# Kernel optimization log

Hardware: AMD Instinct MI355X
Metric: run time of the kernel (lower is better)

Reference implementation:

```python
import jax, jax.numpy as jnp
import numpy as np

W_DIM = 512
IN_CH = 512
OUT_CH = 512
K = 3
PAD = K // 2
LR_MUL = 1.0
WEIGHT_GAIN = LR_MUL / np.sqrt(IN_CH * K * K)
MOD_WEIGHT_GAIN = 1.0 / np.sqrt(W_DIM)  # EqualizedLinear lr_mul=1.0
MOD_BIAS_GAIN = 1.0


def setup_inputs() -> dict:
    key = jax.random.key(0)
    k1, k2, k3, k4 = jax.random.split(key, 4)
    x = jax.random.normal(k1, (16, IN_CH, 64, 64), dtype=jnp.float32)
    w = jax.random.normal(k2, (16, W_DIM), dtype=jnp.float32)
    weight = jax.random.normal(k3, (OUT_CH, IN_CH, K, K), dtype=jnp.float32) / LR_MUL
    mod_weight = jax.random.normal(k4, (IN_CH, W_DIM), dtype=jnp.float32)
    mod_bias = jnp.ones((IN_CH,), dtype=jnp.float32)  # bias_init=1.0
    return {"x": x, "w": w, "weight": weight, "mod_weight": mod_weight, "mod_bias": mod_bias}


def _conv_one(xi, wi):
    # xi: [C_in, H, W], wi: [C_out, C_in, K, K]
    out = jax.lax.conv_general_dilated(
        xi[None], wi, window_strides=(1, 1),
        padding=[(PAD, PAD), (PAD, PAD)],
        dimension_numbers=("NCHW", "OIHW", "NCHW"))
    return out[0]


def reference(x, w, weight, mod_weight, mod_bias):
    # style = EqualizedLinear(w): [B, C_in]
    style = w @ (mod_weight * MOD_WEIGHT_GAIN).T + mod_bias * MOD_BIAS_GAIN
    # modulate weights per-sample: [B, C_out, C_in, K, K]
    wmod = (weight * WEIGHT_GAIN)[None] * style[:, None, :, None, None]
    # demodulate
    demod = jax.lax.rsqrt(jnp.sum(jnp.square(wmod), axis=(2, 3, 4), keepdims=True) + 1e-8)
    wmod = wmod * demod
    # per-sample conv (groups=batch in the original) via vmap
    out = jax.vmap(_conv_one)(x, wmod)  # [B, C_out, H, W]
    return out
```

## Files before the change

### kernel.cpp

```cpp
#include <hip/hip_runtime.h>
#include <hip/hip_bf16.h>

#define IN_CH 512
#define OUT_CH 512
#define HW 64
#define BATCH 16
#define WEIGHT_GAIN 0.014731391274719739f
#define MOD_WEIGHT_GAIN 0.04419417382415922f

#define PAD_W 66
#define XS_PIX_STRIDE 512

typedef __attribute__((ext_vector_type(8))) short frag8;
typedef __attribute__((ext_vector_type(4))) float f32x4;

__global__ void style_kernel(const float* __restrict__ w, const float* __restrict__ mw,
                             const float* __restrict__ mb, float* __restrict__ style) {
    __shared__ float wsh[512];
    const int b = blockIdx.x;
    const int i = threadIdx.x;
    wsh[i] = w[b * 512 + i];
    __syncthreads();
    const float4* row = (const float4*)(mw + i * 512);
    float s = 0.f;
#pragma unroll 4
    for (int j = 0; j < 128; ++j) {
        float4 v = row[j];
        const float* ws = &wsh[j * 4];
        s += v.x * ws[0] + v.y * ws[1] + v.z * ws[2] + v.w * ws[3];
    }
    style[b * 512 + i] = s * MOD_WEIGHT_GAIN + mb[i];
}

__global__ void wprep_kernel(const float* __restrict__ weight, float* __restrict__ wsq,
                             __hip_bfloat16* __restrict__ wbf) {
    const int idx = blockIdx.x * 256 + threadIdx.x;
    const float* wp = weight + idx * 9;
    float s = 0.f;
#pragma unroll
    for (int kk = 0; kk < 9; ++kk) {
        float v = wp[kk];
        s += v * v;
        wbf[kk * 262144 + idx] = __float2bfloat16(v);
    }
    wsq[idx] = s * (WEIGHT_GAIN * WEIGHT_GAIN);
}

__global__ void demod_kernel(const float* __restrict__ style, const float* __restrict__ wsq,
                             float* __restrict__ sc) {
    __shared__ float s2[512];
    const int b = blockIdx.x;
    const int o = threadIdx.x;
    float st = style[b * 512 + o];
    s2[o] = st * st;
    __syncthreads();
    const float4* row = (const float4*)(wsq + o * 512);
    float acc = 0.f;
#pragma unroll 4
    for (int j = 0; j < 128; ++j) {
        float4 v = row[j];
        const float* ss = &s2[j * 4];
        acc += v.x * ss[0] + v.y * ss[1] + v.z * ss[2] + v.w * ss[3];
    }
    sc[b * 512 + o] = rsqrtf(acc + 1e-8f) * WEIGHT_GAIN;
}

__global__ void xs_kernel(const float* __restrict__ x, const float* __restrict__ style,
                          __hip_bfloat16* __restrict__ xsp) {
    __shared__ float tile[64][65];
    const int y = blockIdx.x;
    const int i0 = blockIdx.y * 64;
    const int b = blockIdx.z;
    const int t = threadIdx.x;

    {
        const int ii = t >> 2;
        const int x0 = (t & 3) * 16;
        const float st = style[b * 512 + i0 + ii];
        const float4* s4 = (const float4*)(x + (((size_t)b * 512 + i0 + ii) * 64 + y) * 64 + x0);
#pragma unroll
        for (int k4 = 0; k4 < 4; ++k4) {
            float4 v = s4[k4];
            float* d = &tile[ii][x0 + k4 * 4];
            d[0] = v.x * st; d[1] = v.y * st; d[2] = v.z * st; d[3] = v.w * st;
        }
    }
    __syncthreads();
    {
        const int xx = t >> 2;
        const int j0 = (t & 3) * 16;
        __hip_bfloat16* dst = xsp + (((size_t)b * PAD_W + (y + 1)) * PAD_W + (xx + 1)) * XS_PIX_STRIDE + i0 + j0;
        union { __hip_bfloat16 h[16]; uint4 u[2]; } pk;
#pragma unroll
        for (int k = 0; k < 16; ++k) pk.h[k] = __float2bfloat16(tile[j0 + k][xx]);
        ((uint4*)dst)[0] = pk.u[0];
        ((uint4*)dst)[1] = pk.u[1];
    }
}

__global__ void conv_kernel(const __hip_bfloat16* __restrict__ wbf,
                            const __hip_bfloat16* __restrict__ xsp,
                            const float* __restrict__ sc,
                            float* __restrict__ out) {
    __shared__ __hip_bfloat16 ash[128 * 64];
    __shared__ __hip_bfloat16 bsh[128 * 64];

    const int t = threadIdx.x;
    const int p0 = blockIdx.x * 128;
    const int m0 = blockIdx.y * 128;
    const int b  = blockIdx.z;
    const int y0 = p0 >> 6;

    const int r_base = t >> 3;
    const int s_slot = (t & 7) ^ (r_base & 7);
    const int aoff = (m0 + r_base) * 512 + s_slot * 8;
    int pixoff[4];
#pragma unroll
    for (int q = 0; q < 4; ++q) {
        const int rB = q * 32 + r_base;
        const int yy = y0 + (rB >> 6);
        const int xx = rB & 63;
        pixoff[q] = (((b * PAD_W) + yy) * PAD_W + xx) * XS_PIX_STRIDE + s_slot * 8;
    }

    const int wv = t >> 6;
    const int wm = (wv >> 1) * 64;
    const int wn = (wv & 1) * 64;
    const int lane = t & 63;
    const int ln15 = lane & 15;
    const int quad = lane >> 4;

    f32x4 acc[4][4] = {};

    const short* ashp = (const short*)ash;
    const short* bshp = (const short*)bsh;

    for (int kk = 0; kk < 9; ++kk) {
        const __hip_bfloat16* wsrc = wbf + kk * 262144 + aoff;
        const int shift = ((kk / 3) * PAD_W + (kk % 3)) * XS_PIX_STRIDE;
        const __hip_bfloat16* xbase = xsp + shift;

        for (int c0 = 0; c0 < 512; c0 += 64) {
#pragma unroll
            for (int q = 0; q < 4; ++q) {
                __builtin_amdgcn_global_load_lds(
                    (const __attribute__((address_space(1))) unsigned int*)(wsrc + q * 16384 + c0),
                    (__attribute__((address_space(3))) unsigned int*)((char*)ash + q * 4096 + t * 16),
                    16, 0, 0);
            }
#pragma unroll
            for (int q = 0; q < 4; ++q) {
                __builtin_amdgcn_global_load_lds(
                    (const __attribute__((address_space(1))) unsigned int*)(xbase + pixoff[q] + c0),
                    (__attribute__((address_space(3))) unsigned int*)((char*)bsh + q * 4096 + t * 16),
                    16, 0, 0);
            }
            __syncthreads();

#pragma unroll
            for (int ks = 0; ks < 2; ++ks) {
                const int gq = ks * 4 + quad;
                frag8 af[4], bfr[4];
#pragma unroll
                for (int mt = 0; mt < 4; ++mt) {
                    const int R = wm + mt * 16 + ln15;
                    af[mt] = *(const frag8*)(ashp + R * 64 + ((gq ^ (R & 7)) << 3));
                }
#pragma unroll
                for (int nt = 0; nt < 4; ++nt) {
                    const int R = wn + nt * 16 + ln15;
                    bfr[nt] = *(const frag8*)(bshp + R * 64 + ((gq ^ (R & 7)) << 3));
                }
#pragma unroll
                for (int mt = 0; mt < 4; ++mt)
#pragma unroll
                    for (int nt = 0; nt < 4; ++nt)
                        acc[mt][nt] = __builtin_amdgcn_mfma_f32_16x16x32_bf16(
                            af[mt], bfr[nt], acc[mt][nt], 0, 0, 0);
            }
            __syncthreads();
        }
    }

    const float* scb = sc + b * 512;
    float* outb = out + (size_t)b * 512 * 4096;
#pragma unroll
    for (int mt = 0; mt < 4; ++mt) {
        const int mrow = m0 + wm + mt * 16 + quad * 4;
#pragma unroll
        for (int v = 0; v < 4; ++v) {
            const float s = scb[mrow + v];
            float* orow = outb + (size_t)(mrow + v) * 4096 + p0 + wn + ln15;
#pragma unroll
            for (int nt = 0; nt < 4; ++nt)
                orow[nt * 16] = acc[mt][nt][v] * s;
        }
    }
}

extern "C" void kernel_launch(void* const* d_in, const int* in_sizes, int n_in,
                              void* d_out, int out_size, void* d_ws, size_t ws_size,
                              hipStream_t stream) {
    (void)in_sizes; (void)n_in; (void)out_size; (void)ws_size;
    const float* x      = (const float*)d_in[0];
    const float* w      = (const float*)d_in[1];
    const float* weight = (const float*)d_in[2];
    const float* mw     = (const float*)d_in[3];
    const float* mb     = (const float*)d_in[4];
    float* out = (float*)d_out;

    char* ws = (char*)d_ws;
    float* style         = (float*)(ws + 0);
    float* sc            = (float*)(ws + 32768);
    float* wsq           = (float*)(ws + 65536);
    __hip_bfloat16* wbf  = (__hip_bfloat16*)(ws + 1114112);
    __hip_bfloat16* xsp  = (__hip_bfloat16*)(ws + 5832704);

    hipMemsetAsync(xsp, 0, (size_t)BATCH * PAD_W * PAD_W * XS_PIX_STRIDE * 2, stream);

    style_kernel<<<dim3(BATCH), dim3(512), 0, stream>>>(w, mw, mb, style);
    wprep_kernel<<<dim3(1024), dim3(256), 0, stream>>>(weight, wsq, wbf);
    demod_kernel<<<dim3(BATCH), dim3(512), 0, stream>>>(style, wsq, sc);
    xs_kernel<<<dim3(64, 8, BATCH), dim3(256), 0, stream>>>(x, style, xsp);
    conv_kernel<<<dim3(32, 4, BATCH), dim3(256), 0, stream>>>(wbf, xsp, sc, out);
}
```

Before: 575.8 us.

## Parallelize prep kernels with wave-per-row reductions and zero only padded border

Style and demod matvecs move from 16 blocks (one thread per output row, serial over 512 inputs) to one wavefront per output with shuffle reductions across 2048 blocks, which spreads the work over the whole GPU. The full-buffer memset of the padded activation tensor is replaced by a small kernel that zeroes only the border pixels. The x-scaling transpose kernel drops its shared-memory tile: each lane handles one pixel, reads 32 channels with strided loads and writes 64 contiguous bytes. The prep phase is latency-bound, so the conv kernel still dominates total time, and the strided uncoalesced-per-lane reads in xs_kernel could hurt.

```diff
diff --git a/kernel.cpp b/kernel.cpp
--- a/kernel.cpp
+++ b/kernel.cpp
@@ -16,20 +16,19 @@
 
 __global__ void style_kernel(const float* __restrict__ w, const float* __restrict__ mw,
                              const float* __restrict__ mb, float* __restrict__ style) {
-    __shared__ float wsh[512];
-    const int b = blockIdx.x;
-    const int i = threadIdx.x;
-    wsh[i] = w[b * 512 + i];
-    __syncthreads();
-    const float4* row = (const float4*)(mw + i * 512);
-    float s = 0.f;
-#pragma unroll 4
-    for (int j = 0; j < 128; ++j) {
-        float4 v = row[j];
-        const float* ws = &wsh[j * 4];
-        s += v.x * ws[0] + v.y * ws[1] + v.z * ws[2] + v.w * ws[3];
-    }
-    style[b * 512 + i] = s * MOD_WEIGHT_GAIN + mb[i];
+    const int gw = (blockIdx.x * 256 + threadIdx.x) >> 6;
+    const int lane = threadIdx.x & 63;
+    const int b = gw >> 9;
+    const int i = gw & 511;
+    const float4* mwp = (const float4*)(mw + (size_t)i * 512 + lane * 8);
+    const float4* wp  = (const float4*)(w + (size_t)b * 512 + lane * 8);
+    float4 m0 = mwp[0], m1 = mwp[1];
+    float4 w0 = wp[0],  w1 = wp[1];
+    float s = m0.x * w0.x + m0.y * w0.y + m0.z * w0.z + m0.w * w0.w
+            + m1.x * w1.x + m1.y * w1.y + m1.z * w1.z + m1.w * w1.w;
+#pragma unroll
+    for (int off = 32; off > 0; off >>= 1) s += __shfl_down(s, off, 64);
+    if (lane == 0) style[(size_t)b * 512 + i] = s * MOD_WEIGHT_GAIN + mb[i];
 }
 
 __global__ void wprep_kernel(const float* __restrict__ weight, float* __restrict__ wsq,
@@ -48,54 +47,55 @@
 
 __global__ void demod_kernel(const float* __restrict__ style, const float* __restrict__ wsq,
                              float* __restrict__ sc) {
-    __shared__ float s2[512];
-    const int b = blockIdx.x;
-    const int o = threadIdx.x;
-    float st = style[b * 512 + o];
-    s2[o] = st * st;
-    __syncthreads();
-    const float4* row = (const float4*)(wsq + o * 512);
-    float acc = 0.f;
-#pragma unroll 4
-    for (int j = 0; j < 128; ++j) {
-        float4 v = row[j];
-        const float* ss = &s2[j * 4];
-        acc += v.x * ss[0] + v.y * ss[1] + v.z * ss[2] + v.w * ss[3];
-    }
-    sc[b * 512 + o] = rsqrtf(acc + 1e-8f) * WEIGHT_GAIN;
+    const int gw = (blockIdx.x * 256 + threadIdx.x) >> 6;
+    const int lane = threadIdx.x & 63;
+    const int b = gw >> 9;
+    const int o = gw & 511;
+    const float4* wq = (const float4*)(wsq + (size_t)o * 512 + lane * 8);
+    const float4* st = (const float4*)(style + (size_t)b * 512 + lane * 8);
+    float4 q0 = wq[0], q1 = wq[1];
+    float4 s0 = st[0], s1 = st[1];
+    float acc = q0.x * s0.x * s0.x + q0.y * s0.y * s0.y + q0.z * s0.z * s0.z + q0.w * s0.w * s0.w
+              + q1.x * s1.x * s1.x + q1.y * s1.y * s1.y + q1.z * s1.z * s1.z + q1.w * s1.w * s1.w;
+#pragma unroll
+    for (int off = 32; off > 0; off >>= 1) acc += __shfl_down(acc, off, 64);
+    if (lane == 0) sc[(size_t)b * 512 + o] = rsqrtf(acc + 1e-8f) * WEIGHT_GAIN;
 }
 
 __global__ void xs_kernel(const float* __restrict__ x, const float* __restrict__ style,
                           __hip_bfloat16* __restrict__ xsp) {
-    __shared__ float tile[64][65];
     const int y = blockIdx.x;
-    const int i0 = blockIdx.y * 64;
     const int b = blockIdx.z;
     const int t = threadIdx.x;
-
-    {
-        const int ii = t >> 2;
-        const int x0 = (t & 3) * 16;
-        const float st = style[b * 512 + i0 + ii];
-        const float4* s4 = (const float4*)(x + (((size_t)b * 512 + i0 + ii) * 64 + y) * 64 + x0);
-#pragma unroll
-        for (int k4 = 0; k4 < 4; ++k4) {
-            float4 v = s4[k4];
-            float* d = &tile[ii][x0 + k4 * 4];
-            d[0] = v.x * st; d[1] = v.y * st; d[2] = v.z * st; d[3] = v.w * st;
-        }
-    }
-    __syncthreads();
-    {
-        const int xx = t >> 2;
-        const int j0 = (t & 3) * 16;
-        __hip_bfloat16* dst = xsp + (((size_t)b * PAD_W + (y + 1)) * PAD_W + (xx + 1)) * XS_PIX_STRIDE + i0 + j0;
-        union { __hip_bfloat16 h[16]; uint4 u[2]; } pk;
-#pragma unroll
-        for (int k = 0; k < 16; ++k) pk.h[k] = __float2bfloat16(tile[j0 + k][xx]);
-        ((uint4*)dst)[0] = pk.u[0];
-        ((uint4*)dst)[1] = pk.u[1];
-    }
+    const int lane = t & 63;
+    const int j0 = (blockIdx.y * 4 + (t >> 6)) * 32;
+
+    const float* xb = x + (((size_t)b * 512 + j0) * 64 + y) * 64 + lane;
+    const float* stb = style + (size_t)b * 512 + j0;
+    __hip_bfloat16* dst = xsp + (((size_t)b * PAD_W + (y + 1)) * PAD_W + (lane + 1)) * XS_PIX_STRIDE + j0;
+
+    union { __hip_bfloat16 h[32]; uint4 u[4]; } pk;
+#pragma unroll
+    for (int k = 0; k < 32; ++k) {
+        float v = xb[(size_t)k * 4096];
+        pk.h[k] = __float2bfloat16(v * stb[k]);
+    }
+#pragma unroll
+    for (int q = 0; q < 4; ++q) ((uint4*)dst)[q] = pk.u[q];
+}
+
+__global__ void border_kernel(__hip_bfloat16* __restrict__ xsp) {
+    const int gw = (blockIdx.x * 256 + threadIdx.x) >> 6;
+    const int lane = threadIdx.x & 63;
+    const int b = gw / 260;
+    const int p = gw % 260;
+    int row, col;
+    if (p < 66)       { row = 0;            col = p; }
+    else if (p < 132) { row = 65;           col = p - 66; }
+    else if (p < 196) { row = p - 132 + 1;  col = 0; }
+    else              { row = p - 196 + 1;  col = 65; }
+    uint4* dst = (uint4*)(xsp + (((size_t)b * PAD_W + row) * PAD_W + col) * XS_PIX_STRIDE);
+    dst[lane] = uint4{0, 0, 0, 0};
 }
 
 __global__ void conv_kernel(const __hip_bfloat16* __restrict__ wbf,
@@ -216,11 +216,10 @@
     __hip_bfloat16* wbf  = (__hip_bfloat16*)(ws + 1114112);
     __hip_bfloat16* xsp  = (__hip_bfloat16*)(ws + 5832704);
 
-    hipMemsetAsync(xsp, 0, (size_t)BATCH * PAD_W * PAD_W * XS_PIX_STRIDE * 2, stream);
-
-    style_kernel<<<dim3(BATCH), dim3(512), 0, stream>>>(w, mw, mb, style);
     wprep_kernel<<<dim3(1024), dim3(256), 0, stream>>>(weight, wsq, wbf);
-    demod_kernel<<<dim3(BATCH), dim3(512), 0, stream>>>(style, wsq, sc);
-    xs_kernel<<<dim3(64, 8, BATCH), dim3(256), 0, stream>>>(x, style, xsp);
+    style_kernel<<<dim3(2048), dim3(256), 0, stream>>>(w, mw, mb, style);
+    demod_kernel<<<dim3(2048), dim3(256), 0, stream>>>(style, wsq, sc);
+    border_kernel<<<dim3(1040), dim3(256), 0, stream>>>(xsp);
+    xs_kernel<<<dim3(64, 4, BATCH), dim3(256), 0, stream>>>(x, style, xsp);
     conv_kernel<<<dim3(32, 4, BATCH), dim3(256), 0, stream>>>(wbf, xsp, sc, out);
 }
```

Measured after the change: 526.6 us. 1.09x faster.
